# Performance work log

Hardware: AMD Instinct MI355X
Metric: run time of the kernel (lower is better)

The kernel has to match this reference:

```python
import jax, jax.numpy as jnp
import numpy as np

D_MODEL = 512
N_HEADS = 8
HEAD_DIM = D_MODEL // N_HEADS  # 64


def setup_inputs() -> dict:
    key = jax.random.key(0)
    ks = jax.random.split(key, 12)
    B, SQ, SK = 4, 2048, 2048
    s = 1.0 / np.sqrt(D_MODEL)
    return {
        "query": jax.random.normal(ks[0], (B, SQ, D_MODEL), jnp.float32),
        "key": jax.random.normal(ks[1], (B, SK, D_MODEL), jnp.float32),
        "value": jax.random.normal(ks[2], (B, SK, D_MODEL), jnp.float32),
        "Wq": jax.random.normal(ks[3], (D_MODEL, D_MODEL), jnp.float32) * s,
        "bq": jnp.zeros((D_MODEL,), jnp.float32),
        "Wk": jax.random.normal(ks[4], (D_MODEL, D_MODEL), jnp.float32) * s,
        "bk": jnp.zeros((D_MODEL,), jnp.float32),
        "Wv": jax.random.normal(ks[5], (D_MODEL, D_MODEL), jnp.float32) * s,
        "bv": jnp.zeros((D_MODEL,), jnp.float32),
        "Wo": jax.random.normal(ks[6], (D_MODEL, D_MODEL), jnp.float32) * s,
        "bo": jnp.zeros((D_MODEL,), jnp.float32),
    }


def reference(query, key, value, Wq, bq, Wk, bk, Wv, bv, Wo, bo):
    B, SQ, _ = query.shape
    SK = key.shape[1]
    # QKV projections
    Q = query @ Wq.T + bq  # [B,SQ,D]
    K = key @ Wk.T + bk    # [B,SK,D]
    V = value @ Wv.T + bv  # [B,SK,D]
    # split heads -> [B,H,S,hd]
    Q = Q.reshape(B, SQ, N_HEADS, HEAD_DIM).transpose(0, 2, 1, 3)
    K = K.reshape(B, SK, N_HEADS, HEAD_DIM).transpose(0, 2, 1, 3)
    V = V.reshape(B, SK, N_HEADS, HEAD_DIM).transpose(0, 2, 1, 3)
    scale = jnp.sqrt(jnp.float32(HEAD_DIM))
    scores = jnp.einsum('bhqd,bhkd->bhqk', Q, K) / scale  # [B,H,SQ,SK]
    attn = jax.nn.softmax(scores, axis=-1)  # dropout p=0 (eval)
    ctx = jnp.einsum('bhqk,bhkd->bhqd', attn, V)
    ctx = ctx.transpose(0, 2, 1, 3).reshape(B, SQ, D_MODEL)
    # exact (erf) GELU as in torch F.gelu default
    out = jax.nn.gelu(ctx, approximate=False) @ Wo.T + bo
    return out
```

## Files before the change

kernel.cpp:

```cpp
#include <hip/hip_runtime.h>
#include <hip/hip_bf16.h>

#define D_MODEL 512
#define N_HEADS 8
#define HEAD_DIM 64
#define BATCH 4
#define SEQ 2048

typedef _Float16 f16;
typedef _Float16 f16x8 __attribute__((ext_vector_type(8)));
typedef _Float16 f16x4 __attribute__((ext_vector_type(4)));
typedef float f32x4 __attribute__((ext_vector_type(4)));
typedef unsigned int u32x4 __attribute__((ext_vector_type(4)));

#define MFMA16(a, b, c) __builtin_amdgcn_mfma_f32_16x16x32_f16((a), (b), (c), 0, 0, 0)

#define GLOAD_LDS16(src, dst)                                                   \
    __builtin_amdgcn_global_load_lds(                                           \
        (const __attribute__((address_space(1))) void*)(src),                   \
        (__attribute__((address_space(3))) void*)(dst), 16, 0, 0)

#if __has_builtin(__builtin_amdgcn_exp2f)
#define EXP2(x) __builtin_amdgcn_exp2f(x)
#else
#define EXP2(x) __expf((x) * 0.6931471805599453f)
#endif

#define QSCALE 0.18033688011112042f
#define OFF2 8.656170245333781f

__global__ __launch_bounds__(256) void wsplit(
    const float* __restrict__ w0, const float* __restrict__ w1,
    const float* __restrict__ w2, const float* __restrict__ w3,
    f16* __restrict__ h0, f16* __restrict__ h1,
    f16* __restrict__ h2, f16* __restrict__ h3)
{
    const int j = blockIdx.y;
    const float* s = (j == 0) ? w0 : (j == 1) ? w1 : (j == 2) ? w2 : w3;
    f16* dh = (j == 0) ? h0 : (j == 1) ? h1 : (j == 2) ? h2 : h3;
    const int n4 = (D_MODEL * D_MODEL) >> 2;
    for (int i = blockIdx.x * 256 + threadIdx.x; i < n4; i += gridDim.x * 256) {
        float4 x = ((const float4*)s)[i];
        f16x4 hv = {(f16)x.x, (f16)x.y, (f16)x.z, (f16)x.w};
        ((f16x4*)dh)[i] = hv;
    }
}

__global__ __launch_bounds__(256, 3) void proj_mfma(
    const float* __restrict__ Xq, const float* __restrict__ Xk,
    const float* __restrict__ Xv,
    const f16* __restrict__ Wqh, const f16* __restrict__ Wkh,
    const f16* __restrict__ Wvh,
    const float* __restrict__ bq, const float* __restrict__ bk,
    const float* __restrict__ bv,
    f16* __restrict__ Qh, f16* __restrict__ Kh, f16* __restrict__ Vt)
{
    __shared__ f16 ldsA[128 * 64];
    __shared__ f16 ldsW[128 * 64];

    const int z = blockIdx.z;
    const float* X = (z == 0) ? Xq : (z == 1) ? Xk : Xv;
    const f16* Wh = (z == 0) ? Wqh : (z == 1) ? Wkh : Wvh;
    const float* bias = (z == 0) ? bq : (z == 1) ? bk : bv;

    const int m0 = blockIdx.x * 128;
    const int n0 = blockIdx.y * 128;

    const int tid = threadIdx.x;
    const int w = tid >> 6, l = tid & 63;
    const int lp = l >> 4, lq = l & 15;
    const int wm = w >> 1, wn = w & 1;

    f32x4 acc[4][4] = {};

    for (int kt = 0; kt < D_MODEL; kt += 64) {
        __syncthreads();
        float4 av[4][2];
        int arow[4], aslot[4];
#pragma unroll
        for (int j = 0; j < 4; ++j) {
            const int chunk = j * 256 + tid;
            arow[j] = chunk >> 3;
            aslot[j] = chunk & 7;
            const float* sp = X + (size_t)(m0 + arow[j]) * D_MODEL + kt + aslot[j] * 8;
            av[j][0] = *(const float4*)sp;
            av[j][1] = *(const float4*)(sp + 4);
        }
#pragma unroll
        for (int j = 0; j < 4; ++j) {
            const int cb = j * 256 + w * 64;
            const int chunk = cb + l;
            const int row = chunk >> 3;
            const int slot = (chunk & 7) ^ (row & 7);
            GLOAD_LDS16(Wh + (size_t)(n0 + row) * D_MODEL + kt + slot * 8,
                        ldsW + cb * 8);
        }
#pragma unroll
        for (int j = 0; j < 4; ++j) {
            f16x8 hv;
            hv[0] = (f16)av[j][0].x; hv[1] = (f16)av[j][0].y;
            hv[2] = (f16)av[j][0].z; hv[3] = (f16)av[j][0].w;
            hv[4] = (f16)av[j][1].x; hv[5] = (f16)av[j][1].y;
            hv[6] = (f16)av[j][1].z; hv[7] = (f16)av[j][1].w;
            *(f16x8*)(ldsA + arow[j] * 64 + ((aslot[j] ^ (arow[j] & 7)) << 3)) = hv;
        }
        __syncthreads();

        f16x8 af[4][2];
#pragma unroll
        for (int mt = 0; mt < 4; ++mt) {
            const int R = wm * 64 + mt * 16 + lq;
#pragma unroll
            for (int s = 0; s < 2; ++s)
                af[mt][s] = *(const f16x8*)(ldsA + R * 64 + (((s * 4 + lp) ^ (R & 7)) << 3));
        }
        __builtin_amdgcn_s_setprio(1);
#pragma unroll
        for (int nt = 0; nt < 4; ++nt) {
            const int R = wn * 64 + nt * 16 + lq;
            f16x8 b0 = *(const f16x8*)(ldsW + R * 64 + (((0 + lp) ^ (R & 7)) << 3));
            f16x8 b1 = *(const f16x8*)(ldsW + R * 64 + (((4 + lp) ^ (R & 7)) << 3));
#pragma unroll
            for (int mt = 0; mt < 4; ++mt) {
                acc[mt][nt] = MFMA16(af[mt][0], b0, acc[mt][nt]);
                acc[mt][nt] = MFMA16(af[mt][1], b1, acc[mt][nt]);
            }
        }
        __builtin_amdgcn_s_setprio(0);
    }

    const int m_base = m0 + wm * 64;
    const int n_base = n0 + wn * 64;
    const int b = m0 / SEQ;
    const int h = n_base >> 6;
    const size_t bh_ = (size_t)b * N_HEADS + h;

    if (z == 0) {
#pragma unroll
        for (int nt = 0; nt < 4; ++nt) {
            const int n = n_base + nt * 16 + lq;
            const float bn = bias[n];
            const int d = n & 63;
#pragma unroll
            for (int mt = 0; mt < 4; ++mt) {
#pragma unroll
                for (int r = 0; r < 4; ++r) {
                    const int s = (m_base + mt * 16 + lp * 4 + r) & (SEQ - 1);
                    Qh[(bh_ * SEQ + s) * 64 + d] = (f16)((acc[mt][nt][r] + bn) * QSCALE);
                }
            }
        }
    } else if (z == 1) {
#pragma unroll
        for (int nt = 0; nt < 4; ++nt) {
            const int n = n_base + nt * 16 + lq;
            const float bn = bias[n];
            const int d = n & 63;
#pragma unroll
            for (int mt = 0; mt < 4; ++mt) {
#pragma unroll
                for (int r = 0; r < 4; ++r) {
                    const int s = (m_base + mt * 16 + lp * 4 + r) & (SEQ - 1);
                    Kh[(bh_ * SEQ + s) * 64 + d] = (f16)(acc[mt][nt][r] + bn);
                }
            }
        }
    } else {
#pragma unroll
        for (int nt = 0; nt < 4; ++nt) {
            const int n = n_base + nt * 16 + lq;
            const float bn = bias[n];
            const int d = n & 63;
#pragma unroll
            for (int mt = 0; mt < 4; ++mt) {
                const int s0 = (m_base + mt * 16 + lp * 4) & (SEQ - 1);
                f16x4 col;
#pragma unroll
                for (int r = 0; r < 4; ++r)
                    col[r] = (f16)(acc[mt][nt][r] + bn);
                *(f16x4*)(Vt + (bh_ * 64 + d) * SEQ + s0) = col;
            }
        }
    }
}

__global__ __launch_bounds__(256, 4) void out_mfma(
    const f16* __restrict__ Gh, const f16* __restrict__ Woh,
    const float* __restrict__ bo, float* __restrict__ Out)
{
    __shared__ f16 ldsA[64 * 64];
    __shared__ f16 ldsW[128 * 64];

    const int m0 = blockIdx.x * 64;
    const int n0 = blockIdx.y * 128;

    const int tid = threadIdx.x;
    const int w = tid >> 6, l = tid & 63;
    const int lp = l >> 4, lq = l & 15;
    const int wm = w >> 1, wn = w & 1;

    f32x4 acc[2][4] = {};

    for (int kt = 0; kt < D_MODEL; kt += 64) {
        __syncthreads();
#pragma unroll
        for (int j = 0; j < 2; ++j) {
            const int cb = j * 256 + w * 64;
            const int chunk = cb + l;
            const int row = chunk >> 3;
            const int slot = (chunk & 7) ^ (row & 7);
            GLOAD_LDS16(Gh + (size_t)(m0 + row) * D_MODEL + kt + slot * 8,
                        ldsA + cb * 8);
        }
#pragma unroll
        for (int j = 0; j < 4; ++j) {
            const int cb = j * 256 + w * 64;
            const int chunk = cb + l;
            const int row = chunk >> 3;
            const int slot = (chunk & 7) ^ (row & 7);
            GLOAD_LDS16(Woh + (size_t)(n0 + row) * D_MODEL + kt + slot * 8,
                        ldsW + cb * 8);
        }
        __syncthreads();

        f16x8 af[2][2];
#pragma unroll
        for (int mt = 0; mt < 2; ++mt) {
            const int R = wm * 32 + mt * 16 + lq;
#pragma unroll
            for (int s = 0; s < 2; ++s)
                af[mt][s] = *(const f16x8*)(ldsA + R * 64 + (((s * 4 + lp) ^ (R & 7)) << 3));
        }
        __builtin_amdgcn_s_setprio(1);
#pragma unroll
        for (int nt = 0; nt < 4; ++nt) {
            const int R = wn * 64 + nt * 16 + lq;
            f16x8 b0 = *(const f16x8*)(ldsW + R * 64 + (((0 + lp) ^ (R & 7)) << 3));
            f16x8 b1 = *(const f16x8*)(ldsW + R * 64 + (((4 + lp) ^ (R & 7)) << 3));
#pragma unroll
            for (int mt = 0; mt < 2; ++mt) {
                acc[mt][nt] = MFMA16(af[mt][0], b0, acc[mt][nt]);
                acc[mt][nt] = MFMA16(af[mt][1], b1, acc[mt][nt]);
            }
        }
        __builtin_amdgcn_s_setprio(0);
    }

#pragma unroll
    for (int nt = 0; nt < 4; ++nt) {
        const int n = n0 + wn * 64 + nt * 16 + lq;
        const float bn = bo[n];
#pragma unroll
        for (int mt = 0; mt < 2; ++mt) {
#pragma unroll
            for (int r = 0; r < 4; ++r) {
                const int m = m0 + wm * 32 + mt * 16 + lp * 4 + r;
                Out[(size_t)m * D_MODEL + n] = acc[mt][nt][r] + bn;
            }
        }
    }
}

__global__ __launch_bounds__(256, 2) void flash_mfma(
    const f16* __restrict__ Qh, const f16* __restrict__ Kh,
    const f16* __restrict__ Vt, f16* __restrict__ Gh)
{
    __shared__ f16 KV[2][2][4096];

    const int tid = threadIdx.x;
    const int w  = tid >> 6;
    const int l  = tid & 63;
    const int lp = l >> 4;
    const int lq = l & 15;

    const int id = blockIdx.x;
    const int work = (id & 7) * 64 + (id >> 3);
    const int bh = work >> 4;
    const int b  = bh >> 3, h = bh & 7;
    const int q0 = (work & 15) * 128 + w * 32;

    f16x8 qf[2][2];
#pragma unroll
    for (int sub = 0; sub < 2; ++sub)
#pragma unroll
        for (int s = 0; s < 2; ++s)
            qf[sub][s] = *(const f16x8*)(Qh + ((size_t)bh * SEQ + q0 + sub * 16 + lq) * 64
                                          + s * 32 + lp * 8);

    f16x8 ones;
#pragma unroll
    for (int i = 0; i < 8; ++i) ones[i] = (f16)1.f;

    f32x4 o[2][4];
#pragma unroll
    for (int sub = 0; sub < 2; ++sub)
#pragma unroll
        for (int c = 0; c < 4; ++c) o[sub][c] = (f32x4){0.f, 0.f, 0.f, 0.f};
    f32x4 lf[2] = {(f32x4){0.f, 0.f, 0.f, 0.f}, (f32x4){0.f, 0.f, 0.f, 0.f}};

    auto STAGE = [&](int k0, int bf) {
#pragma unroll
        for (int j = 0; j < 4; ++j) {
            const int gi = w + 4 * j;
            const int tset = gi >> 3;
            const int t = gi & 7;
            const int lrow = t * 8 + (l >> 3);
            const int slot = (l & 7) ^ (lrow & 7);
            if (tset == 0)
                GLOAD_LDS16(Kh + ((size_t)bh * SEQ + k0 + lrow) * 64 + slot * 8,
                            &KV[bf][0][t * 512]);
            else
                GLOAD_LDS16(Vt + ((size_t)bh * 64 + lrow) * SEQ + k0 + slot * 8,
                            &KV[bf][1][t * 512]);
        }
    };

    STAGE(0, 0);
    int buf = 0;
    const int NT = SEQ / 64;

    for (int t = 0; t < NT; ++t) {
        asm volatile("s_waitcnt vmcnt(0)" ::: "memory");
        __builtin_amdgcn_s_barrier();
        if (t < NT - 1) STAGE((t + 1) * 64, buf ^ 1);
        __builtin_amdgcn_sched_barrier(0);

        const f16* Kt_ = &KV[buf][0][0];
        const f16* Vt_ = &KV[buf][1][0];

        f32x4 st[2][4];
#pragma unroll
        for (int sub = 0; sub < 2; ++sub)
#pragma unroll
            for (int c = 0; c < 4; ++c)
                st[sub][c] = (f32x4){-OFF2, -OFF2, -OFF2, -OFF2};
        __builtin_amdgcn_s_setprio(1);
#pragma unroll
        for (int mt = 0; mt < 4; ++mt) {
            const int krow = mt * 16 + lq;
#pragma unroll
            for (int s = 0; s < 2; ++s) {
                const int byteoff = krow * 128 + (((4 * s + lp) ^ (krow & 7)) << 4);
                f16x8 ah = *(const f16x8*)((const char*)Kt_ + byteoff);
#pragma unroll
                for (int sub = 0; sub < 2; ++sub)
                    st[sub][mt] = MFMA16(ah, qf[sub][s], st[sub][mt]);
            }
        }
        __builtin_amdgcn_s_setprio(0);

        f16x8 vbr[2][4];
#pragma unroll
        for (int s = 0; s < 2; ++s)
#pragma unroll
            for (int nt = 0; nt < 4; ++nt) {
                const int d = nt * 16 + lq;
                const int byteoff = d * 128 + (((4 * s + lp) ^ (d & 7)) << 4);
                vbr[s][nt] = *(const f16x8*)((const char*)Vt_ + byteoff);
            }

        f16x8 pa[2][2];
#pragma unroll
        for (int sub = 0; sub < 2; ++sub) {
            unsigned int pk0[4], pk1[4];
#pragma unroll
            for (int mt = 0; mt < 4; ++mt) {
                float e0 = EXP2(st[sub][mt][0]);
                float e1 = EXP2(st[sub][mt][1]);
                float e2 = EXP2(st[sub][mt][2]);
                float e3 = EXP2(st[sub][mt][3]);
                pk0[mt] = __builtin_bit_cast(unsigned int,
                              __builtin_amdgcn_cvt_pkrtz(e0, e1));
                pk1[mt] = __builtin_bit_cast(unsigned int,
                              __builtin_amdgcn_cvt_pkrtz(e2, e3));
            }
#pragma unroll
            for (int s = 0; s < 2; ++s) {
                unsigned int x0 = pk0[2 * s], y0 = pk0[2 * s + 1];
                unsigned int x1 = pk1[2 * s], y1 = pk1[2 * s + 1];
                asm("v_permlane32_swap_b32 %0, %1" : "+v"(x0), "+v"(y0));
                asm("v_permlane16_swap_b32 %0, %1" : "+v"(x0), "+v"(y0));
                asm("v_permlane32_swap_b32 %0, %1" : "+v"(x1), "+v"(y1));
                asm("v_permlane16_swap_b32 %0, %1" : "+v"(x1), "+v"(y1));
                u32x4 t4 = {x0, x1, y0, y1};
                pa[sub][s] = __builtin_bit_cast(f16x8, t4);
            }
        }

        __builtin_amdgcn_s_setprio(1);
#pragma unroll
        for (int s = 0; s < 2; ++s) {
#pragma unroll
            for (int sub = 0; sub < 2; ++sub) {
                lf[sub] = MFMA16(pa[sub][s], ones, lf[sub]);
#pragma unroll
                for (int nt = 0; nt < 4; ++nt)
                    o[sub][nt] = MFMA16(pa[sub][s], vbr[s][nt], o[sub][nt]);
            }
        }
        __builtin_amdgcn_s_setprio(0);

        buf ^= 1;
    }

#pragma unroll
    for (int sub = 0; sub < 2; ++sub) {
#pragma unroll
        for (int j = 0; j < 4; ++j) {
            const float inv = 1.f / lf[sub][j];
            const int row = q0 + sub * 16 + lp * 4 + j;
#pragma unroll
            for (int nt = 0; nt < 4; ++nt) {
                float x = o[sub][nt][j] * inv;
                float g = 0.5f * x * (1.f + erff(x * 0.70710678118654752f));
                Gh[((size_t)(b * SEQ + row)) * D_MODEL + h * 64 + nt * 16 + lq] = (f16)g;
            }
        }
    }
}

extern "C" void kernel_launch(void* const* d_in, const int* in_sizes, int n_in,
                              void* d_out, int out_size, void* d_ws, size_t ws_size,
                              hipStream_t stream)
{
    const float* query = (const float*)d_in[0];
    const float* key   = (const float*)d_in[1];
    const float* value = (const float*)d_in[2];
    const float* Wq = (const float*)d_in[3];
    const float* bq = (const float*)d_in[4];
    const float* Wk = (const float*)d_in[5];
    const float* bk = (const float*)d_in[6];
    const float* Wv = (const float*)d_in[7];
    const float* bv = (const float*)d_in[8];
    const float* Wo = (const float*)d_in[9];
    const float* bo = (const float*)d_in[10];

    char* ws = (char*)d_ws;
    const size_t MB = 1024 * 1024;
    const size_t KB = 1024;
    f16* Qh = (f16*)(ws + 0 * MB);
    f16* Kh = (f16*)(ws + 8 * MB);
    f16* Vt = (f16*)(ws + 16 * MB);
    f16* Gh = (f16*)(ws + 24 * MB);
    f16* Wqh = (f16*)(ws + 32 * MB);
    f16* Wkh = (f16*)(ws + 32 * MB + 512 * KB);
    f16* Wvh = (f16*)(ws + 33 * MB);
    f16* Woh = (f16*)(ws + 33 * MB + 512 * KB);

    wsplit<<<dim3(64, 4), 256, 0, stream>>>(Wq, Wk, Wv, Wo, Wqh, Wkh, Wvh, Woh);

    proj_mfma<<<dim3(BATCH * SEQ / 128, D_MODEL / 128, 3), 256, 0, stream>>>(
        query, key, value, Wqh, Wkh, Wvh, bq, bk, bv, Qh, Kh, Vt);

    flash_mfma<<<dim3(512), 256, 0, stream>>>(Qh, Kh, Vt, Gh);

    out_mfma<<<dim3(BATCH * SEQ / 64, D_MODEL / 128), 256, 0, stream>>>(
        Gh, Woh, bo, (float*)d_out);
}
```

Measured before the change: 85.79 us.

## Software-pipeline attention loop so QK^T of next tile overlaps softmax/PV of current

Splits the attention inner loop into a QK^T stage and a softmax+PV stage and interleaves them across two register sets, so the next tile's score MFMAs and V fragment loads run alongside the exp/permlane/PV work of the previous tile. The loop is manually unrolled by two with ping-pong buffers and a prologue/epilogue. The goal is to hide transcendental and LDS latency behind matrix work. The cost is doubled score and V-fragment registers, which may lower occupancy or cause spills.

```diff
diff --git a/kernel.cpp b/kernel.cpp
--- a/kernel.cpp
+++ b/kernel.cpp
@@ -315,20 +315,9 @@
         }
     };
 
-    STAGE(0, 0);
-    int buf = 0;
-    const int NT = SEQ / 64;
-
-    for (int t = 0; t < NT; ++t) {
-        asm volatile("s_waitcnt vmcnt(0)" ::: "memory");
-        __builtin_amdgcn_s_barrier();
-        if (t < NT - 1) STAGE((t + 1) * 64, buf ^ 1);
-        __builtin_amdgcn_sched_barrier(0);
-
-        const f16* Kt_ = &KV[buf][0][0];
-        const f16* Vt_ = &KV[buf][1][0];
-
-        f32x4 st[2][4];
+    auto QKT = [&](int bf, f32x4 (&st)[2][4], f16x8 (&vbr)[2][4]) {
+        const f16* Kt_ = &KV[bf][0][0];
+        const f16* Vt_ = &KV[bf][1][0];
 #pragma unroll
         for (int sub = 0; sub < 2; ++sub)
 #pragma unroll
@@ -348,8 +337,6 @@
             }
         }
         __builtin_amdgcn_s_setprio(0);
-
-        f16x8 vbr[2][4];
 #pragma unroll
         for (int s = 0; s < 2; ++s)
 #pragma unroll
@@ -358,7 +345,9 @@
                 const int byteoff = d * 128 + (((4 * s + lp) ^ (d & 7)) << 4);
                 vbr[s][nt] = *(const f16x8*)((const char*)Vt_ + byteoff);
             }
-
+    };
+
+    auto SMPV = [&](f32x4 (&st)[2][4], f16x8 (&vbr)[2][4]) {
         f16x8 pa[2][2];
 #pragma unroll
         for (int sub = 0; sub < 2; ++sub) {
@@ -386,7 +375,6 @@
                 pa[sub][s] = __builtin_bit_cast(f16x8, t4);
             }
         }
-
         __builtin_amdgcn_s_setprio(1);
 #pragma unroll
         for (int s = 0; s < 2; ++s) {
@@ -399,9 +387,42 @@
             }
         }
         __builtin_amdgcn_s_setprio(0);
-
-        buf ^= 1;
-    }
+    };
+
+    f32x4 stA[2][4], stB[2][4];
+    f16x8 vbrA[2][4], vbrB[2][4];
+
+    STAGE(0, 0);
+    asm volatile("s_waitcnt vmcnt(0)" ::: "memory");
+    __builtin_amdgcn_s_barrier();
+    STAGE(64, 1);
+    __builtin_amdgcn_sched_barrier(0);
+    QKT(0, stA, vbrA);
+
+#pragma unroll 1
+    for (int tt = 0; tt < 15; ++tt) {
+        const int t1 = 2 * tt + 1;
+        asm volatile("s_waitcnt vmcnt(0)" ::: "memory");
+        __builtin_amdgcn_s_barrier();
+        STAGE((t1 + 1) * 64, 0);
+        __builtin_amdgcn_sched_barrier(0);
+        QKT(1, stB, vbrB);
+        SMPV(stA, vbrA);
+
+        asm volatile("s_waitcnt vmcnt(0)" ::: "memory");
+        __builtin_amdgcn_s_barrier();
+        STAGE((t1 + 2) * 64, 1);
+        __builtin_amdgcn_sched_barrier(0);
+        QKT(0, stA, vbrA);
+        SMPV(stB, vbrB);
+    }
+
+    asm volatile("s_waitcnt vmcnt(0)" ::: "memory");
+    __builtin_amdgcn_s_barrier();
+    __builtin_amdgcn_sched_barrier(0);
+    QKT(1, stB, vbrB);
+    SMPV(stA, vbrA);
+    SMPV(stB, vbrB);
 
 #pragma unroll
     for (int sub = 0; sub < 2; ++sub) {
```

Result: no change. 85.51 us (-0.3%).
